# Kernel tuning notes

Measured on AMD Instinct MI355X. Metric: run time of the kernel, lower is better.

The kernel has to match this reference:

```python
import jax, jax.numpy as jnp
import numpy as np

B, S, DIM = 2, 2048, 4096
NH, NKV, HD = 32, 8, 128  # q heads, kv heads, head dim
ROPE_THETA = 10000.0


def _rope_tables(seq_len, head_dim, dtype=jnp.float32):
    inv = 1.0 / (ROPE_THETA ** (jnp.arange(0, head_dim, 2, dtype=jnp.float32) / head_dim))
    t = jnp.arange(seq_len, dtype=jnp.float32)
    f = jnp.outer(t, inv)  # [S, HD/2]
    return jnp.cos(f).astype(dtype), jnp.sin(f).astype(dtype)


def setup_inputs() -> dict:
    key = jax.random.key(0)
    ks = jax.random.split(key, 5)
    cos, sin = _rope_tables(S, HD)
    scale = 0.02
    return {
        "x": jax.random.normal(ks[0], (B, S, DIM), jnp.float32),
        "start_pos": 0,
        "freqs_cos": cos,
        "freqs_sin": sin,
        "wq": jax.random.normal(ks[1], (DIM, NH * HD), jnp.float32) * scale,
        "wk": jax.random.normal(ks[2], (DIM, NKV * HD), jnp.float32) * scale,
        "wv": jax.random.normal(ks[3], (DIM, NKV * HD), jnp.float32) * scale,
        "wo": jax.random.normal(ks[4], (NH * HD, DIM), jnp.float32) * scale,
    }


def _apply_rope(x, cos, sin):
    # x: [B, S, H, D]; rotate interleaved (even, odd) pairs as complex numbers
    xr, xi = x[..., 0::2], x[..., 1::2]
    c = cos[None, :, None, :]
    s = sin[None, :, None, :]
    out_r = xr * c - xi * s
    out_i = xr * s + xi * c
    return jnp.stack([out_r, out_i], axis=-1).reshape(x.shape)


def reference(x, start_pos, freqs_cos, freqs_sin, wq, wk, wv, wo):
    b, s, _ = x.shape
    n_rep = NH // NKV
    xq = (x @ wq).reshape(b, s, NH, HD)
    xk = (x @ wk).reshape(b, s, NKV, HD)
    xv = (x @ wv).reshape(b, s, NKV, HD)
    xq = _apply_rope(xq, freqs_cos, freqs_sin)
    xk = _apply_rope(xk, freqs_cos, freqs_sin)
    # GQA: group q heads [B,S,NKV,n_rep,HD] against shared kv heads (no repeat_kv materialization)
    xqg = xq.reshape(b, s, NKV, n_rep, HD)
    scale = 1.0 / jnp.sqrt(jnp.asarray(HD, x.dtype))
    scores = jnp.einsum('bqhrd,bkhd->bhrqk', xqg, xk) * scale  # [B,NKV,n_rep,S,S]
    probs = jax.nn.softmax(scores, axis=-1)
    out = jnp.einsum('bhrqk,bkhd->bqhrd', probs, xv)  # [B,S,NKV,n_rep,HD]
    out = out.reshape(b, s, NH * HD)
    return out @ wo
```

## Files before the change

kernel.cpp:

```cpp
#include <hip/hip_runtime.h>

typedef unsigned short u16;
typedef unsigned int   u32;
typedef __attribute__((ext_vector_type(4))) float floatx4;
typedef __attribute__((ext_vector_type(8))) short shortx8;
typedef __attribute__((ext_vector_type(8))) u16   ushortx8;

#define B_   2
#define S_   2048
#define DIM_ 4096
#define NH_  32
#define NKV_ 8
#define HD_  128
#define MTOT (B_*S_)
#define NQKV (NH_*HD_ + 2*NKV_*HD_)
#define QSCALE 0.12753785735803168f
#define KSCALE 1.0f

typedef __attribute__((address_space(3))) u32 lds_u32;
typedef const __attribute__((address_space(1))) u32 gbl_u32;

__device__ inline u16 f2bf(float f) {
  __bf16 h = (__bf16)f;
  return __builtin_bit_cast(u16, h);
}
__device__ inline float bf2f(u16 u) {
  u32 x = ((u32)u) << 16;
  return __builtin_bit_cast(float, x);
}
__device__ inline shortx8 ldfrag(const u16* p) {
  return __builtin_bit_cast(shortx8, *(const uint4*)p);
}

__global__ __launch_bounds__(256) void cvt_f32_bf16(const float* __restrict__ src,
                                                    u16* __restrict__ dst) {
  int i = blockIdx.x * 256 + threadIdx.x;
  const float4* s4 = (const float4*)src;
  float4 a = s4[2*i], c = s4[2*i+1];
  ushortx8 o;
  o[0]=f2bf(a.x); o[1]=f2bf(a.y); o[2]=f2bf(a.z); o[3]=f2bf(a.w);
  o[4]=f2bf(c.x); o[5]=f2bf(c.y); o[6]=f2bf(c.z); o[7]=f2bf(c.w);
  *(ushortx8*)(dst + (size_t)i*8) = o;
}

__global__ __launch_bounds__(256) void transpose_cvt(const float* __restrict__ w,
                                                     u16* __restrict__ wt, int K, int N) {
  __shared__ float tile[32][33];
  int n0 = blockIdx.x * 32, k0 = blockIdx.y * 32;
  int tx = threadIdx.x & 31, ty = threadIdx.x >> 5;
#pragma unroll
  for (int i = 0; i < 4; i++) {
    int r = ty*4 + i;
    tile[r][tx] = w[(size_t)(k0 + r)*N + n0 + tx];
  }
  __syncthreads();
#pragma unroll
  for (int i = 0; i < 4; i++) {
    int n = ty*4 + i;
    wt[(size_t)(n0 + n)*K + k0 + tx] = f2bf(tile[tx][n]);
  }
}

template<int OUT_BF16>
__global__ __launch_bounds__(256) void gemm_bt(const u16* __restrict__ A,
                                               const u16* __restrict__ Bt,
                                               void* __restrict__ Cv,
                                               int M, int N, int K) {
  __shared__ u16 As[128*64];
  __shared__ u16 Bs[128*64];
  const int tid = threadIdx.x;
  const int w = tid >> 6, l = tid & 63, quad = l >> 4, c16 = l & 15;
  const int bm = blockIdx.y * 128, bn = blockIdx.x * 128;
  const int wm = (w & 1) * 64, wn = (w >> 1) * 64;
  const int drow = l >> 3;
  const int gchunk = (l & 7) ^ drow;
  const int dcol = gchunk * 8;
  floatx4 acc[4][4];
#pragma unroll
  for (int mi = 0; mi < 4; mi++)
#pragma unroll
    for (int ni = 0; ni < 4; ni++) acc[mi][ni] = floatx4{0.f,0.f,0.f,0.f};

  for (int k0 = 0; k0 < K; k0 += 64) {
    __syncthreads();
#pragma unroll
    for (int j = 0; j < 4; j++) {
      int row = w*32 + j*8 + drow;
      __builtin_amdgcn_global_load_lds(
          (gbl_u32*)(A + (size_t)(bm + row)*K + k0 + dcol),
          (lds_u32*)(As + (w*32 + j*8)*64), 16, 0, 0);
      __builtin_amdgcn_global_load_lds(
          (gbl_u32*)(Bt + (size_t)(bn + row)*K + k0 + dcol),
          (lds_u32*)(Bs + (w*32 + j*8)*64), 16, 0, 0);
    }
    __syncthreads();
#pragma unroll
    for (int ks = 0; ks < 2; ks++) {
      shortx8 af[4], bfr[4];
#pragma unroll
      for (int mi = 0; mi < 4; mi++) {
        int row = wm + mi*16 + c16;
        int ch  = (ks*4 + quad) ^ (row & 7);
        af[mi] = ldfrag(As + row*64 + ch*8);
      }
#pragma unroll
      for (int ni = 0; ni < 4; ni++) {
        int row = wn + ni*16 + c16;
        int ch  = (ks*4 + quad) ^ (row & 7);
        bfr[ni] = ldfrag(Bs + row*64 + ch*8);
      }
#pragma unroll
      for (int mi = 0; mi < 4; mi++)
#pragma unroll
        for (int ni = 0; ni < 4; ni++)
          acc[mi][ni] = __builtin_amdgcn_mfma_f32_16x16x32_bf16(af[mi], bfr[ni], acc[mi][ni], 0, 0, 0);
    }
  }
#pragma unroll
  for (int mi = 0; mi < 4; mi++)
#pragma unroll
    for (int i = 0; i < 4; i++) {
      int row = bm + wm + mi*16 + quad*4 + i;
#pragma unroll
      for (int ni = 0; ni < 4; ni++) {
        int col = bn + wn + ni*16 + c16;
        float v = acc[mi][ni][i];
        if (OUT_BF16) ((u16*)Cv)[(size_t)row*N + col] = f2bf(v);
        else          ((float*)Cv)[(size_t)row*N + col] = v;
      }
    }
}

__global__ __launch_bounds__(256) void rope_kernel(const u16* __restrict__ qkv,
                                                   const float* __restrict__ fc,
                                                   const float* __restrict__ fs,
                                                   u16* __restrict__ q_r,
                                                   u16* __restrict__ k_r) {
  u32 idx  = blockIdx.x * 256 + threadIdx.x;
  u32 t    = idx & 63;
  u32 rest = idx >> 6;
  u32 m    = rest / 40u;
  u32 hh   = rest - m*40u;
  u32 s    = m & (S_ - 1);
  float c  = fc[s*64 + t], sn = fs[s*64 + t];
  u32 src; u16* dst; u32 dstoff; float scale;
  if (hh < (u32)NH_) {
    src = m*NQKV + hh*HD_ + 2*t;  dst = q_r;  dstoff = m*(NH_*HD_) + hh*HD_ + 2*t;  scale = QSCALE;
  } else {
    u32 hk = hh - NH_;
    src = m*NQKV + NH_*HD_ + hk*HD_ + 2*t;  dst = k_r;  dstoff = m*(NKV_*HD_) + hk*HD_ + 2*t;  scale = KSCALE;
  }
  u32 pair = *(const u32*)(qkv + src);
  float xr = bf2f((u16)(pair & 0xffffu));
  float xi = bf2f((u16)(pair >> 16));
  float orr = (xr*c - xi*sn) * scale;
  float oii = (xr*sn + xi*c) * scale;
  u32 outp = (u32)f2bf(orr) | ((u32)f2bf(oii) << 16);
  *(u32*)(dst + dstoff) = outp;
}

__global__ __launch_bounds__(256) void v_transpose(const u16* __restrict__ qkv,
                                                   u16* __restrict__ vt) {
  __shared__ u16 tile[32][33];
  int bh = blockIdx.y; int b = bh >> 3, hk = bh & 7;
  int ts = (blockIdx.x & 63) * 32;
  int td = (blockIdx.x >> 6) * 32;
  int tx = threadIdx.x & 31, ty = threadIdx.x >> 5;
#pragma unroll
  for (int i = 0; i < 4; i++) {
    int r = ty*4 + i;
    tile[r][tx] = qkv[(size_t)(b*S_ + ts + r)*NQKV + (NH_*HD_ + NKV_*HD_) + hk*HD_ + td + tx];
  }
  __syncthreads();
#pragma unroll
  for (int i = 0; i < 4; i++) {
    int d = ty*4 + i;
    vt[((size_t)bh*HD_ + td + d)*S_ + ts + tx] = tile[tx][d];
  }
}

__global__ __launch_bounds__(256) void attn_kernel(const u16* __restrict__ Q,
                                                   const u16* __restrict__ Kr,
                                                   const u16* __restrict__ Vt,
                                                   u16* __restrict__ Out) {
  __shared__ u16 Qs[64*128];
  __shared__ u16 Ks[2][64*128];
  __shared__ u16 Vts[2][128*64];
  const int tid = threadIdx.x;
  const int w = tid >> 6, l = tid & 63, quad = l >> 4, c16 = l & 15;
  const int qt = blockIdx.x, h = blockIdx.y, b = blockIdx.z;
  const int hk = h >> 2;

  const u16* kbase = Kr + (size_t)(b*S_)*(NKV_*HD_) + hk*HD_;
  const u16* vbase = Vt + (size_t)(b*NKV_ + hk)*HD_*S_;

  {
    const u16* qbase = Q + (size_t)(b*S_ + qt*64)*(NH_*HD_) + h*HD_;
#pragma unroll
    for (int j = 0; j < 4; j++) {
      int rowb = w*16 + j*4;
      int r = rowb + (l >> 4);
      int gch = (l & 15) ^ (r & 7);
      __builtin_amdgcn_global_load_lds(
          (gbl_u32*)(qbase + (size_t)r*(NH_*HD_) + gch*8),
          (lds_u32*)(Qs + rowb*128), 16, 0, 0);
    }
  }
#pragma unroll
  for (int j = 0; j < 4; j++) {
    int rowb = w*16 + j*4;
    int r = rowb + (l >> 4);
    int gch = (l & 15) ^ (r & 7);
    __builtin_amdgcn_global_load_lds(
        (gbl_u32*)(kbase + (size_t)r*(NKV_*HD_) + gch*8),
        (lds_u32*)(Ks[0] + rowb*128), 16, 0, 0);
    int rowbv = w*32 + j*8;
    int rv = rowbv + (l >> 3);
    int gchv = (l & 7) ^ (rv & 7);
    __builtin_amdgcn_global_load_lds(
        (gbl_u32*)(vbase + (size_t)rv*S_ + gchv*8),
        (lds_u32*)(Vts[0] + rowbv*64), 16, 0, 0);
  }
  __syncthreads();

  shortx8 aq[4];
#pragma unroll
  for (int kk = 0; kk < 4; kk++)
    aq[kk] = ldfrag(Qs + (w*16 + c16)*128 + ((kk*4 + quad) ^ (c16 & 7))*8);

  shortx8 vones;
#pragma unroll
  for (int e = 0; e < 8; e++) vones[e] = (short)0x3F80;

  floatx4 o[8];
#pragma unroll
  for (int f = 0; f < 8; f++) o[f] = floatx4{0.f,0.f,0.f,0.f};
  floatx4 lacc = floatx4{0.f,0.f,0.f,0.f};
  float mrow[4] = {-1e30f,-1e30f,-1e30f,-1e30f};
  u16* pw = Qs + (w*16)*128;

  int cur = 0;
  for (int kt = 0; kt < S_/64; kt++) {
    if (kt) __syncthreads();

    if (kt + 1 < S_/64) {
      int nb = cur ^ 1;
#pragma unroll
      for (int j = 0; j < 4; j++) {
        int rowb = w*16 + j*4;
        int r = rowb + (l >> 4);
        int gch = (l & 15) ^ (r & 7);
        __builtin_amdgcn_global_load_lds(
            (gbl_u32*)(kbase + (size_t)((kt+1)*64 + r)*(NKV_*HD_) + gch*8),
            (lds_u32*)(Ks[nb] + rowb*128), 16, 0, 0);
        int rowbv = w*32 + j*8;
        int rv = rowbv + (l >> 3);
        int gchv = (l & 7) ^ (rv & 7);
        __builtin_amdgcn_global_load_lds(
            (gbl_u32*)(vbase + (size_t)rv*S_ + (kt+1)*64 + gchv*8),
            (lds_u32*)(Vts[nb] + rowbv*64), 16, 0, 0);
      }
    }

    floatx4 sc[4];
#pragma unroll
    for (int nt = 0; nt < 4; nt++) sc[nt] = floatx4{0.f,0.f,0.f,0.f};
    __builtin_amdgcn_s_setprio(1);
#pragma unroll
    for (int kk = 0; kk < 4; kk++)
#pragma unroll
      for (int nt = 0; nt < 4; nt++) {
        int rowk = nt*16 + c16;
        shortx8 bk = ldfrag(Ks[cur] + rowk*128 + ((kk*4 + quad) ^ (c16 & 7))*8);
        sc[nt] = __builtin_amdgcn_mfma_f32_16x16x32_bf16(aq[kk], bk, sc[nt], 0, 0, 0);
      }
    __builtin_amdgcn_s_setprio(0);

    float mxall = fmaxf(fmaxf(fmaxf(sc[0][0], sc[0][1]), fmaxf(sc[0][2], sc[0][3])),
                        fmaxf(fmaxf(sc[1][0], sc[1][1]), fmaxf(sc[1][2], sc[1][3])));
    mxall = fmaxf(mxall,
                  fmaxf(fmaxf(fmaxf(sc[2][0], sc[2][1]), fmaxf(sc[2][2], sc[2][3])),
                        fmaxf(fmaxf(sc[3][0], sc[3][1]), fmaxf(sc[3][2], sc[3][3]))));
    mxall = fmaxf(mxall, __shfl_xor(mxall, 1));
    mxall = fmaxf(mxall, __shfl_xor(mxall, 2));
    mxall = fmaxf(mxall, __shfl_xor(mxall, 4));
    mxall = fmaxf(mxall, __shfl_xor(mxall, 8));
    float mlow = fminf(fminf(mrow[0], mrow[1]), fminf(mrow[2], mrow[3]));

    if (__all(mxall - mlow <= 8.0f)) {
#pragma unroll
      for (int i = 0; i < 4; i++)
#pragma unroll
        for (int nt = 0; nt < 4; nt++)
          sc[nt][i] = __builtin_amdgcn_exp2f(sc[nt][i] - mrow[i]);
    } else {
      float alpha[4];
#pragma unroll
      for (int i = 0; i < 4; i++) {
        float mx = fmaxf(fmaxf(sc[0][i], sc[1][i]), fmaxf(sc[2][i], sc[3][i]));
        mx = fmaxf(mx, __shfl_xor(mx, 1));
        mx = fmaxf(mx, __shfl_xor(mx, 2));
        mx = fmaxf(mx, __shfl_xor(mx, 4));
        mx = fmaxf(mx, __shfl_xor(mx, 8));
        float mn = fmaxf(mrow[i], mx);
        alpha[i] = __builtin_amdgcn_exp2f(mrow[i] - mn);
        mrow[i] = mn;
#pragma unroll
        for (int nt = 0; nt < 4; nt++)
          sc[nt][i] = __builtin_amdgcn_exp2f(sc[nt][i] - mn);
      }
#pragma unroll
      for (int f = 0; f < 8; f++)
#pragma unroll
        for (int i = 0; i < 4; i++) o[f][i] *= alpha[i];
#pragma unroll
      for (int i = 0; i < 4; i++) lacc[i] *= alpha[i];
    }

#pragma unroll
    for (int nt = 0; nt < 4; nt++)
#pragma unroll
      for (int i = 0; i < 4; i++) {
        int pr = quad*4 + i;
        int ch = (nt*2 + (c16 >> 3)) ^ (pr & 7);
        pw[pr*128 + ch*8 + (c16 & 7)] = f2bf(sc[nt][i]);
      }
    asm volatile("s_waitcnt lgkmcnt(0)" ::: "memory");

    __builtin_amdgcn_s_setprio(1);
#pragma unroll
    for (int kk2 = 0; kk2 < 2; kk2++) {
      shortx8 pf = ldfrag(pw + c16*128 + ((kk2*4 + quad) ^ (c16 & 7))*8);
      lacc = __builtin_amdgcn_mfma_f32_16x16x32_bf16(pf, vones, lacc, 0, 0, 0);
#pragma unroll
      for (int f = 0; f < 8; f++) {
        int rv = f*16 + c16;
        shortx8 vf = ldfrag(Vts[cur] + rv*64 + ((kk2*4 + quad) ^ (rv & 7))*8);
        o[f] = __builtin_amdgcn_mfma_f32_16x16x32_bf16(pf, vf, o[f], 0, 0, 0);
      }
    }
    __builtin_amdgcn_s_setprio(0);
    cur ^= 1;
  }

#pragma unroll
  for (int i = 0; i < 4; i++) {
    int srow = qt*64 + w*16 + quad*4 + i;
    float inv = 1.f / lacc[i];
    size_t base = (size_t)(b*S_ + srow)*(NH_*HD_) + h*HD_;
#pragma unroll
    for (int f = 0; f < 8; f++)
      Out[base + f*16 + c16] = f2bf(o[f][i] * inv);
  }
}

extern "C" void kernel_launch(void* const* d_in, const int* in_sizes, int n_in,
                              void* d_out, int out_size, void* d_ws, size_t ws_size,
                              hipStream_t stream) {
  (void)in_sizes; (void)n_in; (void)out_size; (void)ws_size;
  const float* x  = (const float*)d_in[0];
  const float* fc = (const float*)d_in[2];
  const float* fs = (const float*)d_in[3];
  const float* wq = (const float*)d_in[4];
  const float* wk = (const float*)d_in[5];
  const float* wv = (const float*)d_in[6];
  const float* wo = (const float*)d_in[7];
  float* out = (float*)d_out;

  char* ws = (char*)d_ws;
  u16* xb    = (u16*)(ws);
  u16* wallt = (u16*)(ws + 33554432ull);
  u16* q_r   = (u16*)(ws + 33554432ull);
  u16* k_r   = (u16*)(ws + 67108864ull);
  u16* vt    = (u16*)(ws + 75497472ull);
  u16* wot   = (u16*)(ws + 83886080ull);
  u16* qkvp  = (u16*)(ws + 117440512ull);

  cvt_f32_bf16<<<8192, 256, 0, stream>>>(x, xb);
  transpose_cvt<<<dim3(128,128), 256, 0, stream>>>(wq, wallt, 4096, 4096);
  transpose_cvt<<<dim3(32,128),  256, 0, stream>>>(wk, wallt + (size_t)4096*4096, 4096, 1024);
  transpose_cvt<<<dim3(32,128),  256, 0, stream>>>(wv, wallt + (size_t)5120*4096, 4096, 1024);
  transpose_cvt<<<dim3(128,128), 256, 0, stream>>>(wo, wot, 4096, 4096);

  gemm_bt<1><<<dim3(48,32), 256, 0, stream>>>(xb, wallt, qkvp, MTOT, NQKV, DIM_);

  rope_kernel<<<40960, 256, 0, stream>>>(qkvp, fc, fs, q_r, k_r);
  v_transpose<<<dim3(256,16), 256, 0, stream>>>(qkvp, vt);

  attn_kernel<<<dim3(32,32,2), 256, 0, stream>>>(q_r, k_r, vt, xb);

  gemm_bt<0><<<dim3(32,32), 256, 0, stream>>>(xb, wot, out, MTOT, DIM_, 4096);
}
```

Before: 908.7 us.

## Transpose attention MFMAs so P stays in registers instead of LDS

Swaps the MFMA operand order so scores come out as S^T, with each lane owning one query row. The P fragment for the PV MFMA is then assembled in registers through cross-lane shuffles instead of a round trip through LDS. Row max and row sum become per-lane values reduced with two shuffles each, which removes the ones-vector MFMA used for the sum and the Q LDS buffer (Q is now loaded straight from global into registers). The output is written with packed 64-bit stores. In exchange the shuffles add VALU work and Q loads become uncoalesced per-lane reads.

Result: no change. 925.7 us (+1.9%).

```diff
diff --git a/kernel.cpp b/kernel.cpp
--- a/kernel.cpp
+++ b/kernel.cpp
@@ -2,9 +2,11 @@
 
 typedef unsigned short u16;
 typedef unsigned int   u32;
+typedef unsigned long long u64;
 typedef __attribute__((ext_vector_type(4))) float floatx4;
 typedef __attribute__((ext_vector_type(8))) short shortx8;
 typedef __attribute__((ext_vector_type(8))) u16   ushortx8;
+typedef __attribute__((ext_vector_type(4))) u32   uintx4;
 
 #define B_   2
 #define S_   2048
@@ -183,7 +185,6 @@
                                                    const u16* __restrict__ Kr,
                                                    const u16* __restrict__ Vt,
                                                    u16* __restrict__ Out) {
-  __shared__ u16 Qs[64*128];
   __shared__ u16 Ks[2][64*128];
   __shared__ u16 Vts[2][128*64];
   const int tid = threadIdx.x;
@@ -194,18 +195,14 @@
   const u16* kbase = Kr + (size_t)(b*S_)*(NKV_*HD_) + hk*HD_;
   const u16* vbase = Vt + (size_t)(b*NKV_ + hk)*HD_*S_;
 
+  shortx8 aq[4];
   {
-    const u16* qbase = Q + (size_t)(b*S_ + qt*64)*(NH_*HD_) + h*HD_;
-#pragma unroll
-    for (int j = 0; j < 4; j++) {
-      int rowb = w*16 + j*4;
-      int r = rowb + (l >> 4);
-      int gch = (l & 15) ^ (r & 7);
-      __builtin_amdgcn_global_load_lds(
-          (gbl_u32*)(qbase + (size_t)r*(NH_*HD_) + gch*8),
-          (lds_u32*)(Qs + rowb*128), 16, 0, 0);
-    }
-  }
+    const u16* qrow = Q + (size_t)(b*S_ + qt*64 + w*16 + c16)*(NH_*HD_) + h*HD_;
+#pragma unroll
+    for (int kk = 0; kk < 4; kk++)
+      aq[kk] = ldfrag(qrow + kk*32 + quad*8);
+  }
+
 #pragma unroll
   for (int j = 0; j < 4; j++) {
     int rowb = w*16 + j*4;
@@ -223,21 +220,10 @@
   }
   __syncthreads();
 
-  shortx8 aq[4];
-#pragma unroll
-  for (int kk = 0; kk < 4; kk++)
-    aq[kk] = ldfrag(Qs + (w*16 + c16)*128 + ((kk*4 + quad) ^ (c16 & 7))*8);
-
-  shortx8 vones;
-#pragma unroll
-  for (int e = 0; e < 8; e++) vones[e] = (short)0x3F80;
-
   floatx4 o[8];
 #pragma unroll
   for (int f = 0; f < 8; f++) o[f] = floatx4{0.f,0.f,0.f,0.f};
-  floatx4 lacc = floatx4{0.f,0.f,0.f,0.f};
-  float mrow[4] = {-1e30f,-1e30f,-1e30f,-1e30f};
-  u16* pw = Qs + (w*16)*128;
+  float m = -1e30f, lsum = 0.f;
 
   int cur = 0;
   for (int kt = 0; kt < S_/64; kt++) {
@@ -264,93 +250,104 @@
 
     floatx4 sc[4];
 #pragma unroll
-    for (int nt = 0; nt < 4; nt++) sc[nt] = floatx4{0.f,0.f,0.f,0.f};
+    for (int kb = 0; kb < 4; kb++) sc[kb] = floatx4{0.f,0.f,0.f,0.f};
     __builtin_amdgcn_s_setprio(1);
 #pragma unroll
     for (int kk = 0; kk < 4; kk++)
 #pragma unroll
-      for (int nt = 0; nt < 4; nt++) {
-        int rowk = nt*16 + c16;
-        shortx8 bk = ldfrag(Ks[cur] + rowk*128 + ((kk*4 + quad) ^ (c16 & 7))*8);
-        sc[nt] = __builtin_amdgcn_mfma_f32_16x16x32_bf16(aq[kk], bk, sc[nt], 0, 0, 0);
+      for (int kb = 0; kb < 4; kb++) {
+        int rowk = kb*16 + c16;
+        shortx8 kf = ldfrag(Ks[cur] + rowk*128 + ((kk*4 + quad) ^ (c16 & 7))*8);
+        sc[kb] = __builtin_amdgcn_mfma_f32_16x16x32_bf16(kf, aq[kk], sc[kb], 0, 0, 0);
       }
     __builtin_amdgcn_s_setprio(0);
 
-    float mxall = fmaxf(fmaxf(fmaxf(sc[0][0], sc[0][1]), fmaxf(sc[0][2], sc[0][3])),
-                        fmaxf(fmaxf(sc[1][0], sc[1][1]), fmaxf(sc[1][2], sc[1][3])));
-    mxall = fmaxf(mxall,
-                  fmaxf(fmaxf(fmaxf(sc[2][0], sc[2][1]), fmaxf(sc[2][2], sc[2][3])),
-                        fmaxf(fmaxf(sc[3][0], sc[3][1]), fmaxf(sc[3][2], sc[3][3]))));
-    mxall = fmaxf(mxall, __shfl_xor(mxall, 1));
-    mxall = fmaxf(mxall, __shfl_xor(mxall, 2));
-    mxall = fmaxf(mxall, __shfl_xor(mxall, 4));
-    mxall = fmaxf(mxall, __shfl_xor(mxall, 8));
-    float mlow = fminf(fminf(mrow[0], mrow[1]), fminf(mrow[2], mrow[3]));
-
-    if (__all(mxall - mlow <= 8.0f)) {
-#pragma unroll
-      for (int i = 0; i < 4; i++)
-#pragma unroll
-        for (int nt = 0; nt < 4; nt++)
-          sc[nt][i] = __builtin_amdgcn_exp2f(sc[nt][i] - mrow[i]);
+    float mx = fmaxf(fmaxf(fmaxf(sc[0][0], sc[0][1]), fmaxf(sc[0][2], sc[0][3])),
+                     fmaxf(fmaxf(sc[1][0], sc[1][1]), fmaxf(sc[1][2], sc[1][3])));
+    mx = fmaxf(mx, fmaxf(fmaxf(fmaxf(sc[2][0], sc[2][1]), fmaxf(sc[2][2], sc[2][3])),
+                         fmaxf(fmaxf(sc[3][0], sc[3][1]), fmaxf(sc[3][2], sc[3][3]))));
+    mx = fmaxf(mx, __shfl_xor(mx, 16));
+    mx = fmaxf(mx, __shfl_xor(mx, 32));
+
+    float rs = 0.f;
+    if (__all(mx - m <= 8.0f)) {
+#pragma unroll
+      for (int kb = 0; kb < 4; kb++)
+#pragma unroll
+        for (int i = 0; i < 4; i++) {
+          float p = __builtin_amdgcn_exp2f(sc[kb][i] - m);
+          sc[kb][i] = p; rs += p;
+        }
     } else {
-      float alpha[4];
-#pragma unroll
-      for (int i = 0; i < 4; i++) {
-        float mx = fmaxf(fmaxf(sc[0][i], sc[1][i]), fmaxf(sc[2][i], sc[3][i]));
-        mx = fmaxf(mx, __shfl_xor(mx, 1));
-        mx = fmaxf(mx, __shfl_xor(mx, 2));
-        mx = fmaxf(mx, __shfl_xor(mx, 4));
-        mx = fmaxf(mx, __shfl_xor(mx, 8));
-        float mn = fmaxf(mrow[i], mx);
-        alpha[i] = __builtin_amdgcn_exp2f(mrow[i] - mn);
-        mrow[i] = mn;
-#pragma unroll
-        for (int nt = 0; nt < 4; nt++)
-          sc[nt][i] = __builtin_amdgcn_exp2f(sc[nt][i] - mn);
-      }
-#pragma unroll
-      for (int f = 0; f < 8; f++)
-#pragma unroll
-        for (int i = 0; i < 4; i++) o[f][i] *= alpha[i];
-#pragma unroll
-      for (int i = 0; i < 4; i++) lacc[i] *= alpha[i];
-    }
-
-#pragma unroll
-    for (int nt = 0; nt < 4; nt++)
-#pragma unroll
-      for (int i = 0; i < 4; i++) {
-        int pr = quad*4 + i;
-        int ch = (nt*2 + (c16 >> 3)) ^ (pr & 7);
-        pw[pr*128 + ch*8 + (c16 & 7)] = f2bf(sc[nt][i]);
-      }
-    asm volatile("s_waitcnt lgkmcnt(0)" ::: "memory");
+      float mn = fmaxf(m, mx);
+      float al = __builtin_amdgcn_exp2f(m - mn);
+      m = mn;
+#pragma unroll
+      for (int kb = 0; kb < 4; kb++)
+#pragma unroll
+        for (int i = 0; i < 4; i++) {
+          float p = __builtin_amdgcn_exp2f(sc[kb][i] - mn);
+          sc[kb][i] = p; rs += p;
+        }
+      lsum *= al;
+#pragma unroll
+      for (int f = 0; f < 8; f++) o[f] *= al;
+    }
+    rs += __shfl_xor(rs, 16);
+    rs += __shfl_xor(rs, 32);
+    lsum += rs;
+
+    u32 pk[4][2];
+#pragma unroll
+    for (int kb = 0; kb < 4; kb++)
+#pragma unroll
+      for (int j = 0; j < 2; j++)
+        pk[kb][j] = (u32)f2bf(sc[kb][2*j]) | ((u32)f2bf(sc[kb][2*j+1]) << 16);
+
+#pragma unroll
+    for (int kh = 0; kh < 2; kh++)
+#pragma unroll
+      for (int j = 0; j < 2; j++) {
+        u32 tr = (quad >= 2) ? pk[kh*2][j] : pk[kh*2+1][j];
+        tr = (u32)__shfl_xor((int)tr, 32);
+        if (quad >= 2) pk[kh*2][j] = tr; else pk[kh*2+1][j] = tr;
+      }
+#pragma unroll
+    for (int kh = 0; kh < 2; kh++)
+#pragma unroll
+      for (int j = 0; j < 2; j++) {
+        u32 tr = (quad & 1) ? pk[kh*2][j] : pk[kh*2+1][j];
+        tr = (u32)__shfl_xor((int)tr, 16);
+        if (quad & 1) pk[kh*2][j] = tr; else pk[kh*2+1][j] = tr;
+      }
 
     __builtin_amdgcn_s_setprio(1);
 #pragma unroll
     for (int kk2 = 0; kk2 < 2; kk2++) {
-      shortx8 pf = ldfrag(pw + c16*128 + ((kk2*4 + quad) ^ (c16 & 7))*8);
-      lacc = __builtin_amdgcn_mfma_f32_16x16x32_bf16(pf, vones, lacc, 0, 0, 0);
+      shortx8 pf = __builtin_bit_cast(shortx8,
+          uintx4{pk[2*kk2][0], pk[2*kk2][1], pk[2*kk2+1][0], pk[2*kk2+1][1]});
 #pragma unroll
       for (int f = 0; f < 8; f++) {
         int rv = f*16 + c16;
         shortx8 vf = ldfrag(Vts[cur] + rv*64 + ((kk2*4 + quad) ^ (rv & 7))*8);
-        o[f] = __builtin_amdgcn_mfma_f32_16x16x32_bf16(pf, vf, o[f], 0, 0, 0);
+        o[f] = __builtin_amdgcn_mfma_f32_16x16x32_bf16(vf, pf, o[f], 0, 0, 0);
       }
     }
     __builtin_amdgcn_s_setprio(0);
     cur ^= 1;
   }
 
-#pragma unroll
-  for (int i = 0; i < 4; i++) {
-    int srow = qt*64 + w*16 + quad*4 + i;
-    float inv = 1.f / lacc[i];
-    size_t base = (size_t)(b*S_ + srow)*(NH_*HD_) + h*HD_;
-#pragma unroll
-    for (int f = 0; f < 8; f++)
-      Out[base + f*16 + c16] = f2bf(o[f][i] * inv);
+  {
+    float inv = 1.f / lsum;
+    size_t base = (size_t)(b*S_ + qt*64 + w*16 + c16)*(NH_*HD_) + h*HD_ + quad*4;
+#pragma unroll
+    for (int f = 0; f < 8; f++) {
+      u64 pkd = (u64)f2bf(o[f][0]*inv)
+              | ((u64)f2bf(o[f][1]*inv) << 16)
+              | ((u64)f2bf(o[f][2]*inv) << 32)
+              | ((u64)f2bf(o[f][3]*inv) << 48);
+      *(u64*)(Out + base + f*16) = pkd;
+    }
   }
 }
 
```
